# Kernel optimization log

Hardware: AMD Instinct MI355X
Metric: run time of the kernel (lower is better)

Reference implementation:

```python
import jax, jax.numpy as jnp
import numpy as np

NUM_HEADS = 16
HEAD_DIM = 64
MAX_POS = 2048  # max_position_embeddings


def setup_inputs() -> dict:
    key = jax.random.key(0)
    ks = jax.random.split(key, 8)
    B, S, H = 4, 1024, 1024
    s = 1.0 / np.sqrt(H)
    return {
        "hidden_states": jax.random.normal(ks[0], (B, S, H), jnp.float32),
        "attention_mask": jnp.zeros((B, 1, 1, S), jnp.float32),
        "Wq": jax.random.normal(ks[1], (H, H), jnp.float32) * s,
        "bq": jnp.zeros((H,), jnp.float32),
        "Wk": jax.random.normal(ks[2], (H, H), jnp.float32) * s,
        "bk": jnp.zeros((H,), jnp.float32),
        "Wv": jax.random.normal(ks[3], (H, H), jnp.float32) * s,
        "bv": jnp.zeros((H,), jnp.float32),
        "dist_emb": jax.random.normal(ks[4], (2 * MAX_POS - 1, HEAD_DIM), jnp.float32) * 0.02,
    }


def _split_heads(x):
    B, S, _ = x.shape
    return x.reshape(B, S, NUM_HEADS, HEAD_DIM).transpose(0, 2, 1, 3)  # [B,H,S,dh]


def reference(hidden_states, attention_mask, Wq, bq, Wk, bk, Wv, bv, dist_emb):
    B, S, _ = hidden_states.shape
    q = _split_heads(hidden_states @ Wq + bq)
    k = _split_heads(hidden_states @ Wk + bk)
    v = _split_heads(hidden_states @ Wv + bv)

    scores = jnp.einsum("bhld,bhrd->bhlr", q, k)

    # relative_key_query positional bias
    pos = jnp.arange(S)
    distance = pos[:, None] - pos[None, :]                 # [S,S]
    pe = dist_emb[distance + MAX_POS - 1]                   # [S,S,dh]
    scores = scores + jnp.einsum("bhld,lrd->bhlr", q, pe)
    scores = scores + jnp.einsum("bhrd,lrd->bhlr", k, pe)

    scores = scores / np.sqrt(HEAD_DIM).astype(np.float32)
    scores = scores + attention_mask                        # additive mask broadcast
    probs = jax.nn.softmax(scores, axis=-1)                 # dropout is identity in eval

    ctx = jnp.einsum("bhlr,bhrd->bhld", probs, v)
    ctx = ctx.transpose(0, 2, 1, 3).reshape(B, S, NUM_HEADS * HEAD_DIM)
    return ctx
```

## Files before the change

kernel.cpp:

```cpp
#include <hip/hip_runtime.h>
#include <hip/hip_bf16.h>

typedef __hip_bfloat16 bf16;
typedef __attribute__((ext_vector_type(8))) short bf16x8;
typedef __attribute__((ext_vector_type(4))) float f32x4;
typedef __attribute__((ext_vector_type(2))) unsigned int u32x2;

#define MFMA(a, b, c) __builtin_amdgcn_mfma_f32_16x16x32_bf16((a), (b), (c), 0, 0, 0)

static __device__ __forceinline__ float bf2f(bf16 b) { return __bfloat162float(b); }

static __device__ __forceinline__ unsigned pk2(float a, float b) {
    return __builtin_amdgcn_perm(__builtin_bit_cast(unsigned, b),
                                 __builtin_bit_cast(unsigned, a), 0x07060302u);
}

static __device__ __forceinline__ void gload16(const void* g, void* l) {
    __builtin_amdgcn_global_load_lds(
        (const __attribute__((address_space(1))) void*)g,
        (__attribute__((address_space(3))) void*)l, 16, 0, 0);
}

static __device__ __forceinline__ float quad_max(float x) {
    x = fmaxf(x, __shfl_xor(x, 16));
    x = fmaxf(x, __shfl_xor(x, 32));
    return x;
}
static __device__ __forceinline__ float quad_sum(float x) {
    x += __shfl_xor(x, 16);
    x += __shfl_xor(x, 32);
    return x;
}

__global__ void prep_convert(const float* __restrict__ X, const float* __restrict__ DE,
                             bf16* __restrict__ Xb, bf16* __restrict__ DEb) {
    int i = blockIdx.x * blockDim.x + threadIdx.x;
    if (i < 1048576) {
        float4 v = reinterpret_cast<const float4*>(X)[i];
        bf16* d = Xb + 4 * i;
        d[0] = __float2bfloat16(v.x); d[1] = __float2bfloat16(v.y);
        d[2] = __float2bfloat16(v.z); d[3] = __float2bfloat16(v.w);
    } else {
        int j = i - 1048576;
        if (j < 65520) {
            float4 v = reinterpret_cast<const float4*>(DE)[j];
            bf16* d = DEb + 4 * j;
            d[0] = __float2bfloat16(v.x); d[1] = __float2bfloat16(v.y);
            d[2] = __float2bfloat16(v.z); d[3] = __float2bfloat16(v.w);
        }
    }
}

__global__ void prep_transpose_w(const float* __restrict__ Wq, const float* __restrict__ Wk,
                                 const float* __restrict__ Wv, bf16* __restrict__ WTb) {
    const float* W = (blockIdx.z == 0) ? Wq : (blockIdx.z == 1) ? Wk : Wv;
    bf16* WT = WTb + (size_t)blockIdx.z * (1024u * 1024u);
    __shared__ float t[64][65];
    int tid = threadIdx.x;
    int col = tid & 63;
    int r4 = tid >> 6;
    int i0 = blockIdx.x * 64, o0 = blockIdx.y * 64;
    for (int it = 0; it < 16; ++it) {
        int row = it * 4 + r4;
        t[row][col] = W[(size_t)(i0 + row) * 1024 + o0 + col];
    }
    __syncthreads();
    for (int it = 0; it < 16; ++it) {
        int row = it * 4 + r4;
        WT[(size_t)(o0 + row) * 1024 + i0 + col] = __float2bfloat16(t[col][row]);
    }
}

__global__ __launch_bounds__(256, 2) void proj_gemm(
    const bf16* __restrict__ Xb, const bf16* __restrict__ WTb,
    const float* __restrict__ bq, const float* __restrict__ bk, const float* __restrict__ bv,
    bf16* __restrict__ Qb, bf16* __restrict__ Kb, bf16* __restrict__ VTb) {
    int proj = blockIdx.z;
    const bf16* W = WTb + (size_t)proj * (1024u * 1024u);
    const float* bias = (proj == 0) ? bq : (proj == 1) ? bk : bv;

    __shared__ bf16 XT[128][72];
    __shared__ bf16 WTt[128][72];

    int tid = threadIdx.x;
    int w = tid >> 6, lane = tid & 63, g = lane >> 4, li = lane & 15;
    int wr = w >> 1, wc = w & 1;
    int m0 = blockIdx.x * 128, n0 = blockIdx.y * 128;

    f32x4 acc[4][4];
    for (int mt = 0; mt < 4; mt++)
        for (int nt = 0; nt < 4; nt++) acc[mt][nt] = {0.f, 0.f, 0.f, 0.f};

    for (int ks = 0; ks < 16; ++ks) {
        for (int it = 0; it < 4; ++it) {
            int idx = tid + 256 * it;
            int row = idx >> 3, c = (idx & 7) * 8;
            *reinterpret_cast<bf16x8*>(&XT[row][c]) =
                *reinterpret_cast<const bf16x8*>(Xb + (size_t)(m0 + row) * 1024 + ks * 64 + c);
            *reinterpret_cast<bf16x8*>(&WTt[row][c]) =
                *reinterpret_cast<const bf16x8*>(W + (size_t)(n0 + row) * 1024 + ks * 64 + c);
        }
        __syncthreads();
        for (int kk = 0; kk < 2; ++kk) {
            bf16x8 af[4], bfr[4];
            for (int mt = 0; mt < 4; mt++)
                af[mt] = *reinterpret_cast<const bf16x8*>(&XT[64 * wr + 16 * mt + li][32 * kk + 8 * g]);
            for (int nt = 0; nt < 4; nt++)
                bfr[nt] = *reinterpret_cast<const bf16x8*>(&WTt[64 * wc + 16 * nt + li][32 * kk + 8 * g]);
            for (int mt = 0; mt < 4; mt++)
                for (int nt = 0; nt < 4; nt++)
                    acc[mt][nt] = MFMA(af[mt], bfr[nt], acc[mt][nt]);
        }
        __syncthreads();
    }

    for (int mt = 0; mt < 4; mt++)
        for (int nt = 0; nt < 4; nt++) {
            int n = n0 + 64 * wc + 16 * nt + li;
            int h = n >> 6, d = n & 63;
            float bv_ = bias[n];
            for (int r = 0; r < 4; r++) {
                int m = m0 + 64 * wr + 16 * mt + 4 * g + r;
                int b = m >> 10, s = m & 1023;
                bf16 o = __float2bfloat16(acc[mt][nt][r] + bv_);
                if (proj == 0)      Qb[((size_t)(b * 16 + h) * 1024 + s) * 64 + d] = o;
                else if (proj == 1) Kb[((size_t)(b * 16 + h) * 1024 + s) * 64 + d] = o;
                else                VTb[((size_t)(b * 16 + h) * 64 + d) * 1024 + s] = o;
            }
        }
}

__global__ __launch_bounds__(256, 3) void attn_fused(
    const bf16* __restrict__ Qg, const bf16* __restrict__ Kg,
    const bf16* __restrict__ VTg, const bf16* __restrict__ DEb,
    const float* __restrict__ mask, float* __restrict__ out) {
    const int S = 1024, D = 64;
    const float C8 = 0.18033688011112042f;
    int p_ = blockIdx.x;
    int bh = (p_ & 7) * 8 + ((p_ >> 3) >> 4);
    int qb = (p_ >> 3) & 15;
    int b = bh >> 4, h = bh & 15;
    int L0 = qb * 64;

    int tid = threadIdx.x;
    int w = tid >> 6, lane = tid & 63, g = lane >> 4, li = lane & 15;

    __shared__ __align__(16) char smem[53760];
    float (*M_lds)[64] = reinterpret_cast<float(*)[64]>(smem + 53248);

    const bf16* Qh = Qg + (size_t)bh * S * D;
    const bf16* Kh = Kg + (size_t)bh * S * D;
    const bf16* Vh = VTg + (size_t)bh * D * S;
    const float* maskb = mask + (size_t)b * S;

    int sw = (li & 7) << 4;
    int c0 = (16 * g) ^ sw;
    int c1 = (64 + 16 * g) ^ sw;
    const char* KbL = smem + li * 128;
    const char* KaL = smem + (16 * (3 - w) + li) * 128;
    const char* Vb_ = smem + 8192 + li * 128;
    const char* Db_ = smem + 16384;

    int cr = lane >> 3;
    int sc = 16 * ((lane & 7) ^ cr);

    bf16x8 qa0, qa1;
    {
        const bf16* qrow = Qh + (size_t)(L0 + 16 * w + li) * D;
        qa0 = *reinterpret_cast<const bf16x8*>(qrow + 8 * g);
        qa1 = *reinterpret_cast<const bf16x8*>(qrow + 32 + 8 * g);
    }

    const char* qdb = smem + 32768 + 2560 * w + 162 * li - 8 * g;
    const char* kdb = smem + 43008 + 632 * g + 32 * w + 2 * li + 30;
    char* qsp = smem + 32768 + 2560 * w + 160 * li + 8 * g;
    char* ksp = smem + 43008 + 160 * (48 - 16 * w + li) + 8 * g;
    char* Pp  = smem + 32768 + 2560 * w + 144 * li;

    int de00 = L0 + 1984;
    {
        #pragma unroll
        for (int i = 0; i < 2; ++i) {
            int blk = w * 2 + i;
            int row = blk * 8 + cr;
            gload16((const char*)Kh + (size_t)row * 128 + sc, smem + blk * 1024);
            gload16((const char*)Vh + (size_t)row * 2048 + sc, smem + 8192 + blk * 1024);
        }
        #pragma unroll
        for (int i = 0; i < 4; ++i) {
            int blk = w * 4 + i;
            int row = blk * 8 + cr;
            int ldsoff = (((de00 & 64) * 128) + blk * 1024) & 16383;
            gload16((const char*)DEb + (size_t)(de00 + row) * 128 + sc, smem + 16384 + ldsoff);
        }
        if (tid < 64) M_lds[0][tid] = maskb[tid];
    }

    f32x4 acc_o[4];
    for (int dt = 0; dt < 4; dt++) acc_o[dt] = {0.f, 0.f, 0.f, 0.f};
    float m_run = -1e30f, l_run = 0.f;

    __syncthreads();

    for (int kt = 0; kt < 16; ++kt) {
        int r0 = kt * 64;
        int de0 = de00 - r0;
        bool has_next = (kt < 15);

        if (kt) {
            #pragma unroll
            for (int i = 0; i < 2; ++i) {
                int blk = w * 2 + i;
                int row = blk * 8 + cr;
                gload16((const char*)Vh + (size_t)row * 2048 + (size_t)r0 * 2 + sc,
                        smem + 8192 + blk * 1024);
            }
        }

        __builtin_amdgcn_s_setprio(1);
        f32x4 s_acc[4];
        #pragma unroll
        for (int nt = 0; nt < 4; ++nt) {
            bf16x8 kb0 = *reinterpret_cast<const bf16x8*>(KbL + nt * 2048 + c0);
            bf16x8 kb1 = *reinterpret_cast<const bf16x8*>(KbL + nt * 2048 + c1);
            f32x4 z = {0.f, 0.f, 0.f, 0.f};
            z = MFMA(kb0, qa0, z);
            z = MFMA(kb1, qa1, z);
            s_acc[nt] = z;
        }
        {
            bf16x8 ka0 = *reinterpret_cast<const bf16x8*>(KaL + c0);
            bf16x8 ka1 = *reinterpret_cast<const bf16x8*>(KaL + c1);
            #pragma unroll
            for (int jt = 0; jt < 5; ++jt) {
                int dr = (de0 + 16 * w + 16 * jt + li) & 127;
                bf16x8 d0 = *reinterpret_cast<const bf16x8*>(Db_ + dr * 128 + c0);
                bf16x8 d1 = *reinterpret_cast<const bf16x8*>(Db_ + dr * 128 + c1);
                f32x4 aq = {0.f, 0.f, 0.f, 0.f};
                aq = MFMA(d0, qa0, aq);
                aq = MFMA(d1, qa1, aq);
                f32x4 ak = {0.f, 0.f, 0.f, 0.f};
                ak = MFMA(d0, ka0, ak);
                ak = MFMA(d1, ka1, ak);
                u32x2 uq = {pk2(aq[0], aq[1]), pk2(aq[2], aq[3])};
                *reinterpret_cast<u32x2*>(qsp + 32 * jt) = uq;
                u32x2 uk = {pk2(ak[0], ak[1]), pk2(ak[2], ak[3])};
                *reinterpret_cast<u32x2*>(ksp + 32 * jt) = uk;
            }
        }
        __builtin_amdgcn_s_setprio(0);
        __syncthreads();

        float sM;
        if (has_next) {
            int r0n = r0 + 64;
            int dlo = de0 - 64;
            #pragma unroll
            for (int i = 0; i < 2; ++i) {
                int blk = w * 2 + i;
                int row = blk * 8 + cr;
                gload16((const char*)Kh + (size_t)(r0n + row) * 128 + sc, smem + blk * 1024);
                gload16((const char*)DEb + (size_t)(dlo + row) * 128 + sc,
                        smem + 16384 + (dlo & 64) * 128 + blk * 1024);
            }
            if (tid < 64) sM = maskb[r0n + tid];
        }

        float u[4][4];
        float lmax = -1e30f;
        #pragma unroll
        for (int nt = 0; nt < 4; ++nt) {
            f32x4 mk4 = *reinterpret_cast<const f32x4*>(&M_lds[kt & 1][16 * nt + 4 * g]);
            #pragma unroll
            for (int r = 0; r < 4; ++r) {
                float qd = bf2f(*reinterpret_cast<const bf16*>(qdb + (126 - 32 * nt - 2 * r)));
                float kd = bf2f(*reinterpret_cast<const bf16*>(kdb + (2560 * nt + 158 * r)));
                float uu = s_acc[nt][r] + qd + kd;
                uu = __builtin_fmaf(mk4[r], 8.0f, uu);
                u[nt][r] = uu;
                lmax = fmaxf(lmax, uu);
            }
        }
        float tm = quad_max(lmax);
        bool noskip = !__all(tm <= m_run);
        float scl = 1.0f;
        if (noskip) {
            float mnew = fmaxf(m_run, tm);
            scl = exp2f((m_run - mnew) * C8);
            m_run = mnew;
        }
        float nmc = -m_run * C8;
        float pv[4][4];
        #pragma unroll
        for (int nt = 0; nt < 4; ++nt)
            #pragma unroll
            for (int r = 0; r < 4; ++r)
                pv[nt][r] = exp2f(__builtin_fmaf(u[nt][r], C8, nmc));
        float t0 = (pv[0][0] + pv[0][1]) + (pv[0][2] + pv[0][3]);
        float t1 = (pv[1][0] + pv[1][1]) + (pv[1][2] + pv[1][3]);
        float t2 = (pv[2][0] + pv[2][1]) + (pv[2][2] + pv[2][3]);
        float t3 = (pv[3][0] + pv[3][1]) + (pv[3][2] + pv[3][3]);
        float qs = quad_sum((t0 + t1) + (t2 + t3));
        if (noskip) {
            l_run = l_run * scl + qs;
            #pragma unroll
            for (int dt = 0; dt < 4; dt++) acc_o[dt] *= scl;
        } else {
            l_run += qs;
        }

        #pragma unroll
        for (int nt = 0; nt < 4; ++nt) {
            u32x2 pp = {pk2(pv[nt][0], pv[nt][1]), pk2(pv[nt][2], pv[nt][3])};
            *reinterpret_cast<u32x2*>(Pp + 32 * nt + 8 * g) = pp;
        }
        bf16x8 pb0 = *reinterpret_cast<const bf16x8*>(Pp + 16 * g);
        bf16x8 pb1 = *reinterpret_cast<const bf16x8*>(Pp + 64 + 16 * g);

        __builtin_amdgcn_s_setprio(1);
        #pragma unroll
        for (int dt = 0; dt < 4; dt++) {
            bf16x8 va0 = *reinterpret_cast<const bf16x8*>(Vb_ + dt * 2048 + c0);
            bf16x8 va1 = *reinterpret_cast<const bf16x8*>(Vb_ + dt * 2048 + c1);
            acc_o[dt] = MFMA(va0, pb0, acc_o[dt]);
            acc_o[dt] = MFMA(va1, pb1, acc_o[dt]);
        }
        __builtin_amdgcn_s_setprio(0);

        if (has_next && tid < 64) M_lds[(kt + 1) & 1][tid] = sM;
        __syncthreads();
    }

    float inv = 1.0f / l_run;
    float (*OT)[68] = reinterpret_cast<float (*)[68]>(smem);
    #pragma unroll
    for (int dt = 0; dt < 4; dt++)
        #pragma unroll
        for (int r = 0; r < 4; r++)
            OT[16 * w + li][16 * dt + 4 * g + r] = acc_o[dt][r] * inv;
    __syncthreads();
    {
        int q = tid >> 2, seg = tid & 3;
        float* gout = out + ((size_t)(b * 1024 + L0 + q)) * 1024 + h * 64 + 16 * seg;
        #pragma unroll
        for (int j = 0; j < 4; ++j)
            *reinterpret_cast<float4*>(gout + 4 * j) =
                *reinterpret_cast<const float4*>(&OT[q][16 * seg + 4 * j]);
    }
}

extern "C" void kernel_launch(void* const* d_in, const int* in_sizes, int n_in,
                              void* d_out, int out_size, void* d_ws, size_t ws_size,
                              hipStream_t stream) {
    const float* X   = (const float*)d_in[0];
    const float* msk = (const float*)d_in[1];
    const float* Wq  = (const float*)d_in[2];
    const float* bq  = (const float*)d_in[3];
    const float* Wk  = (const float*)d_in[4];
    const float* bk  = (const float*)d_in[5];
    const float* Wv  = (const float*)d_in[6];
    const float* bv  = (const float*)d_in[7];
    const float* DE  = (const float*)d_in[8];
    float* out = (float*)d_out;

    bf16* ws  = (bf16*)d_ws;
    bf16* Xb  = ws;
    bf16* WTb = ws + 4194304;
    bf16* DEb = ws + 7340032;
    bf16* Qb  = ws + 7602176;
    bf16* Kb  = ws + 11796480;
    bf16* VTb = ws + 15990784;

    prep_convert<<<4352, 256, 0, stream>>>(X, DE, Xb, DEb);
    prep_transpose_w<<<dim3(16, 16, 3), 256, 0, stream>>>(Wq, Wk, Wv, WTb);
    proj_gemm<<<dim3(32, 8, 3), 256, 0, stream>>>(Xb, WTb, bq, bk, bv, Qb, Kb, VTb);
    attn_fused<<<dim3(1024), 256, 0, stream>>>(Qb, Kb, VTb, DEb, msk, out);
}
```

Measured before the change: 160.0 us.

## Double attention query tile to 128 rows per 512-thread block

The attention kernel now processes 128 query rows per block with 8 waves instead of 64 rows with 4 waves. K, V and distance-embedding tiles are shared across twice as many queries, and the distance embeddings sit in a 192-row ring buffer. Each thread now issues one load per tile instead of two or four, and the mask is stored in LDS as bf16. The block uses more LDS (about 80KB), which limits how many blocks fit per CU, and the grid halves to 512 blocks. Storing the mask in bf16 can lose precision for mask values that are not exactly representable.

Measured after the change: 141.5 us. 11.6% less time.

```diff
diff --git a/kernel.cpp b/kernel.cpp
--- a/kernel.cpp
+++ b/kernel.cpp
@@ -130,70 +130,67 @@
         }
 }
 
-__global__ __launch_bounds__(256, 3) void attn_fused(
+__global__ __launch_bounds__(512, 4) void attn_fused(
     const bf16* __restrict__ Qg, const bf16* __restrict__ Kg,
     const bf16* __restrict__ VTg, const bf16* __restrict__ DEb,
     const float* __restrict__ mask, float* __restrict__ out) {
     const int S = 1024, D = 64;
     const float C8 = 0.18033688011112042f;
     int p_ = blockIdx.x;
-    int bh = (p_ & 7) * 8 + ((p_ >> 3) >> 4);
-    int qb = (p_ >> 3) & 15;
+    int idx = p_ >> 3;
+    int bh = (p_ & 7) * 8 + (idx >> 3);
+    int qb = idx & 7;
     int b = bh >> 4, h = bh & 15;
-    int L0 = qb * 64;
+    int L0 = qb * 128;
 
     int tid = threadIdx.x;
     int w = tid >> 6, lane = tid & 63, g = lane >> 4, li = lane & 15;
 
-    __shared__ __align__(16) char smem[53760];
-    float (*M_lds)[64] = reinterpret_cast<float(*)[64]>(smem + 53248);
-
-    const bf16* Qh = Qg + (size_t)bh * S * D;
-    const bf16* Kh = Kg + (size_t)bh * S * D;
-    const bf16* Vh = VTg + (size_t)bh * D * S;
+    __shared__ __align__(16) char smem[81664];
+    bf16 (*Mb)[64] = reinterpret_cast<bf16(*)[64]>(smem + 81408);
+
+    const char* Kh = (const char*)(Kg + (size_t)bh * S * D);
+    const char* Vh = (const char*)(VTg + (size_t)bh * D * S);
+    const char* DEc = (const char*)DEb;
     const float* maskb = mask + (size_t)b * S;
 
     int sw = (li & 7) << 4;
     int c0 = (16 * g) ^ sw;
     int c1 = (64 + 16 * g) ^ sw;
     const char* KbL = smem + li * 128;
-    const char* KaL = smem + (16 * (3 - w) + li) * 128;
+    int gsel = (w < 4) ? (3 - w) : (7 - w);
+    const char* KaL = smem + (16 * gsel + li) * 128;
     const char* Vb_ = smem + 8192 + li * 128;
     const char* Db_ = smem + 16384;
 
-    int cr = lane >> 3;
-    int sc = 16 * ((lane & 7) ^ cr);
+    int srow = tid >> 3;
+    int sc = 16 * ((lane & 7) ^ (lane >> 3));
 
     bf16x8 qa0, qa1;
     {
-        const bf16* qrow = Qh + (size_t)(L0 + 16 * w + li) * D;
+        const bf16* qrow = Qg + (size_t)bh * S * D + (size_t)(L0 + 16 * w + li) * D;
         qa0 = *reinterpret_cast<const bf16x8*>(qrow + 8 * g);
         qa1 = *reinterpret_cast<const bf16x8*>(qrow + 32 + 8 * g);
     }
 
-    const char* qdb = smem + 32768 + 2560 * w + 162 * li - 8 * g;
-    const char* kdb = smem + 43008 + 632 * g + 32 * w + 2 * li + 30;
-    char* qsp = smem + 32768 + 2560 * w + 160 * li + 8 * g;
-    char* ksp = smem + 43008 + 160 * (48 - 16 * w + li) + 8 * g;
-    char* Pp  = smem + 32768 + 2560 * w + 144 * li;
+    const char* qdb = smem + 40960 + 2688 * w + 170 * li - 8 * g;
+    const char* kdb = smem + 62464 + 1176 * g + 32 * w + 2 * li + 30;
+    char* qsp = smem + 40960 + 2688 * w + 168 * li + 8 * g;
+    char* ksp = smem + 62464 + 296 * (16 * gsel + li) + ((w < 4) ? 0 : 128) + 8 * g;
+    char* Pp  = smem + 40960 + 2688 * w + 144 * li;
 
     int de00 = L0 + 1984;
+    int jb = de00 % 192;
     {
-        #pragma unroll
-        for (int i = 0; i < 2; ++i) {
-            int blk = w * 2 + i;
-            int row = blk * 8 + cr;
-            gload16((const char*)Kh + (size_t)row * 128 + sc, smem + blk * 1024);
-            gload16((const char*)Vh + (size_t)row * 2048 + sc, smem + 8192 + blk * 1024);
-        }
-        #pragma unroll
-        for (int i = 0; i < 4; ++i) {
-            int blk = w * 4 + i;
-            int row = blk * 8 + cr;
-            int ldsoff = (((de00 & 64) * 128) + blk * 1024) & 16383;
-            gload16((const char*)DEb + (size_t)(de00 + row) * 128 + sc, smem + 16384 + ldsoff);
-        }
-        if (tid < 64) M_lds[0][tid] = maskb[tid];
+        gload16(Kh + (size_t)srow * 128 + sc, smem + w * 1024);
+        gload16(Vh + (size_t)srow * 2048 + sc, smem + 8192 + w * 1024);
+        #pragma unroll
+        for (int c = 0; c < 3; ++c) {
+            int pb = jb + 64 * c; if (pb >= 192) pb -= 192;
+            gload16(DEc + (size_t)(de00 + 64 * c + srow) * 128 + sc,
+                    smem + 16384 + pb * 128 + w * 1024);
+        }
+        if (tid < 64) Mb[0][tid] = __float2bfloat16(maskb[tid]);
     }
 
     f32x4 acc_o[4];
@@ -204,17 +201,11 @@
 
     for (int kt = 0; kt < 16; ++kt) {
         int r0 = kt * 64;
-        int de0 = de00 - r0;
         bool has_next = (kt < 15);
+        int jbw = jb + 16 * w;
 
         if (kt) {
-            #pragma unroll
-            for (int i = 0; i < 2; ++i) {
-                int blk = w * 2 + i;
-                int row = blk * 8 + cr;
-                gload16((const char*)Vh + (size_t)row * 2048 + (size_t)r0 * 2 + sc,
-                        smem + 8192 + blk * 1024);
-            }
+            gload16(Vh + (size_t)srow * 2048 + (size_t)r0 * 2 + sc, smem + 8192 + w * 1024);
         }
 
         __builtin_amdgcn_s_setprio(1);
@@ -233,9 +224,11 @@
             bf16x8 ka1 = *reinterpret_cast<const bf16x8*>(KaL + c1);
             #pragma unroll
             for (int jt = 0; jt < 5; ++jt) {
-                int dr = (de0 + 16 * w + 16 * jt + li) & 127;
-                bf16x8 d0 = *reinterpret_cast<const bf16x8*>(Db_ + dr * 128 + c0);
-                bf16x8 d1 = *reinterpret_cast<const bf16x8*>(Db_ + dr * 128 + c1);
+                int x = jbw + 16 * jt + li;
+                if (x >= 192) x -= 192;
+                const char* dp = Db_ + x * 128;
+                bf16x8 d0 = *reinterpret_cast<const bf16x8*>(dp + c0);
+                bf16x8 d1 = *reinterpret_cast<const bf16x8*>(dp + c1);
                 f32x4 aq = {0.f, 0.f, 0.f, 0.f};
                 aq = MFMA(d0, qa0, aq);
                 aq = MFMA(d1, qa1, aq);
@@ -254,29 +247,29 @@
         float sM;
         if (has_next) {
             int r0n = r0 + 64;
-            int dlo = de0 - 64;
-            #pragma unroll
-            for (int i = 0; i < 2; ++i) {
-                int blk = w * 2 + i;
-                int row = blk * 8 + cr;
-                gload16((const char*)Kh + (size_t)(r0n + row) * 128 + sc, smem + blk * 1024);
-                gload16((const char*)DEb + (size_t)(dlo + row) * 128 + sc,
-                        smem + 16384 + (dlo & 64) * 128 + blk * 1024);
-            }
+            int dlo = de00 - 64 * (kt + 1);
+            int jbN = (jb >= 64) ? jb - 64 : jb + 128;
+            gload16(Kh + (size_t)(r0n + srow) * 128 + sc, smem + w * 1024);
+            gload16(DEc + (size_t)(dlo + srow) * 128 + sc,
+                    smem + 16384 + jbN * 128 + w * 1024);
             if (tid < 64) sM = maskb[r0n + tid];
+            jb = jbN;
         }
 
         float u[4][4];
         float lmax = -1e30f;
         #pragma unroll
         for (int nt = 0; nt < 4; ++nt) {
-            f32x4 mk4 = *reinterpret_cast<const f32x4*>(&M_lds[kt & 1][16 * nt + 4 * g]);
+            unsigned long long mraw =
+                *reinterpret_cast<const unsigned long long*>(&Mb[kt & 1][16 * nt + 4 * g]);
             #pragma unroll
             for (int r = 0; r < 4; ++r) {
                 float qd = bf2f(*reinterpret_cast<const bf16*>(qdb + (126 - 32 * nt - 2 * r)));
-                float kd = bf2f(*reinterpret_cast<const bf16*>(kdb + (2560 * nt + 158 * r)));
+                float kd = bf2f(*reinterpret_cast<const bf16*>(kdb + (4736 * nt + 294 * r)));
+                float mk = __builtin_bit_cast(float,
+                    (unsigned)((mraw >> (16 * r)) & 0xffffull) << 16);
                 float uu = s_acc[nt][r] + qd + kd;
-                uu = __builtin_fmaf(mk4[r], 8.0f, uu);
+                uu = __builtin_fmaf(mk, 8.0f, uu);
                 u[nt][r] = uu;
                 lmax = fmaxf(lmax, uu);
             }
@@ -327,7 +320,7 @@
         }
         __builtin_amdgcn_s_setprio(0);
 
-        if (has_next && tid < 64) M_lds[(kt + 1) & 1][tid] = sM;
+        if (has_next && tid < 64) Mb[(kt + 1) & 1][tid] = __float2bfloat16(sM);
         __syncthreads();
     }
 
@@ -374,5 +367,5 @@
     prep_convert<<<4352, 256, 0, stream>>>(X, DE, Xb, DEb);
     prep_transpose_w<<<dim3(16, 16, 3), 256, 0, stream>>>(Wq, Wk, Wv, WTb);
     proj_gemm<<<dim3(32, 8, 3), 256, 0, stream>>>(Xb, WTb, bq, bk, bv, Qb, Kb, VTb);
-    attn_fused<<<dim3(1024), 256, 0, stream>>>(Qb, Kb, VTb, DEb, msk, out);
-}
+    attn_fused<<<512, 512, 0, stream>>>(Qb, Kb, VTb, DEb, msk, out);
+}
```
